# Performance work log

Hardware: AMD Instinct MI355X
Metric: run time of the kernel (lower is better)

The kernel has to match this reference:

```python
import jax, jax.numpy as jnp
import numpy as np
from jax import lax

BETA = 0.1
N_CLUSTERS = 64


def setup_inputs() -> dict:
    key = jax.random.key(0)
    ks = jax.random.split(key, 10)
    L, B, Hin, H = 200, 2048, 64, 256
    s = lambda k, shape, scale=0.05: jax.random.normal(k, shape, dtype=jnp.float32) * scale
    return {
        "X": jax.random.normal(ks[0], (L, B, Hin), dtype=jnp.float32),
        "W_ih0": s(ks[1], (4 * H, Hin)),
        "W_hh0": s(ks[2], (4 * H, H)),
        "b_ih0": s(ks[3], (4 * H,)),
        "b_hh0": s(ks[4], (4 * H,)),
        "W_ih1": s(ks[5], (4 * H, H)),
        "W_hh1": s(ks[6], (4 * H, H)),
        "b_ih1": s(ks[7], (4 * H,)),
        "b_hh1": s(ks[8], (4 * H,)),
        "clusters": jax.random.normal(ks[9], (N_CLUSTERS, H), dtype=jnp.float32),
    }


def _lstm_layer(x, W_ih, W_hh, b_ih, b_hh):
    # x: (L, B, I) -> outputs (L, B, H); torch gate order i, f, g, o
    H = W_hh.shape[1]
    B = x.shape[1]
    b = b_ih + b_hh

    def step(carry, xt):
        h, c = carry
        gates = xt @ W_ih.T + h @ W_hh.T + b  # (B, 4H)
        i, f, g, o = jnp.split(gates, 4, axis=-1)
        c = jax.nn.sigmoid(f) * c + jax.nn.sigmoid(i) * jnp.tanh(g)
        h = jax.nn.sigmoid(o) * jnp.tanh(c)
        return (h, c), h

    h0 = jnp.zeros((B, H), x.dtype)
    (_, _), ys = lax.scan(step, (h0, h0), x)
    return ys


def _encode(X, W_ih0, W_hh0, b_ih0, b_hh0, W_ih1, W_hh1, b_ih1, b_hh1):
    y0 = _lstm_layer(X, W_ih0, W_hh0, b_ih0, b_hh0)
    y1 = _lstm_layer(y0, W_ih1, W_hh1, b_ih1, b_hh1)
    return y1[-1]  # latent_X: (B, H), last timestep of top layer


def reference(X, W_ih0, W_hh0, b_ih0, b_hh0, W_ih1, W_hh1, b_ih1, b_hh1, clusters):
    latent_X = _encode(X, W_ih0, W_hh0, b_ih0, b_hh0, W_ih1, W_hh1, b_ih1, b_hh1)

    # kmeans assignment on detached latents (l2 distance)
    lat_sg = lax.stop_gradient(latent_X)
    d2 = (jnp.sum(lat_sg * lat_sg, -1, keepdims=True)
          - 2.0 * lat_sg @ clusters.T
          + jnp.sum(clusters * clusters, -1))  # (B, K)
    cluster_id = jnp.argmin(d2, axis=-1)  # (B,)

    # centroid update from assigned (detached) points; keep old centroid if empty
    sums = jax.ops.segment_sum(lat_sg, cluster_id, num_segments=N_CLUSTERS)
    counts = jax.ops.segment_sum(jnp.ones((lat_sg.shape[0],), lat_sg.dtype),
                                 cluster_id, num_segments=N_CLUSTERS)
    upd = jnp.where(counts[:, None] > 0, sums / jnp.maximum(counts, 1.0)[:, None], clusters)

    # vectorized per-sample cluster distance loss: sum_i 0.5*beta*||latent_i - c[id_i]||^2
    diff = latent_X - upd[cluster_id]  # gather (B, H)
    dist_loss = 0.5 * BETA * jnp.sum(diff * diff)
    return latent_X, dist_loss
```

## Files before the change

kernel.cpp:

```cpp
#include <hip/hip_runtime.h>
#include <hip/hip_bf16.h>
#include <math.h>

typedef unsigned short u16;
typedef unsigned int u32;
typedef __attribute__((ext_vector_type(8))) __bf16 bf16x8;
typedef __attribute__((ext_vector_type(4))) float f32x4;

#define LSTM_L 200
#define LSTM_B 2048
#define LSTM_HIN 64
#define LSTM_H 256
#define NCLUST 64
#define HALF_BETA 0.05f
#define LDS_BYTES 65536
#define ASSIGN_LDS 135424
#define ASSIGN_BLOCKS 64

__device__ __forceinline__ void gload_lds16(const void* g, void* l) {
    __builtin_amdgcn_global_load_lds(
        (__attribute__((address_space(1))) const void*)g,
        (__attribute__((address_space(3))) void*)l, 16, 0, 0);
}

__device__ __forceinline__ float fast_sigmoid(float x) {
    return __builtin_amdgcn_rcpf(1.f + __expf(-x));
}
__device__ __forceinline__ float fast_tanh(float x) {
    return 2.f * __builtin_amdgcn_rcpf(1.f + __expf(-2.f * x)) - 1.f;
}
__device__ __forceinline__ void wt_store(u32* p, u32 v) {
    __hip_atomic_store(p, v, __ATOMIC_RELAXED, __HIP_MEMORY_SCOPE_AGENT);
}

template<int KIN>
__global__ __launch_bounds__(256) void pack_frag(
    const float* __restrict__ Wih, const float* __restrict__ Whh,
    u16* __restrict__ Wp)
{
    constexpr int NCH = (KIN + LSTM_H) / 32;
    const int total = 1024 * (KIN + LSTM_H);
    for (int i = blockIdx.x * 256 + threadIdx.x; i < total; i += gridDim.x * 256) {
        const int e = i & 7;
        int t = i >> 3;
        const int lane = t & 63; t >>= 6;
        const int nf = t & 1;    t >>= 1;
        const int ch = t % NCH;  t /= NCH;
        const int wn = t & 3;
        const int nb = t >> 2;
        const int l15 = lane & 15;
        const int j = (2 * nf + (l15 & 1)) * 256 + nb * 32 + wn * 8 + (l15 >> 1);
        const int k = ch * 32 + ((lane >> 4) << 3) + e;
        const float v = (k < KIN) ? Wih[(size_t)j * KIN + k]
                                  : Whh[(size_t)j * LSTM_H + (k - KIN)];
        Wp[i] = __builtin_bit_cast(u16, (__bf16)v);
    }
}

template<int KIN>
__device__ __forceinline__ void run_layer64(
    const float* __restrict__ xf32,
    const u16* __restrict__ hbelow,
    const u16* __restrict__ hself,
    const u16* __restrict__ Wp,
    const float* __restrict__ bih, const float* __restrict__ bhh,
    u16* __restrict__ hout, float* __restrict__ latout,
    float* __restrict__ cst,
    int blk, char* smem, int tid)
{
    constexpr int NCH = (KIN + LSTM_H) / 32;
    constexpr bool IS_L0 = (KIN == 64);
    const int lane = tid & 63;
    const int wn = tid >> 6;
    const int l15 = lane & 15;
    const int q = lane >> 4;
    const int mb = blk >> 3;
    const int nb = blk & 7;
    const int b0 = mb * 64;

    bf16x8 Breg[NCH][2];
    {
        const u16* wp = Wp + (size_t)((nb * 4 + wn) * NCH) * 1024 + lane * 8;
#pragma unroll
        for (int ch = 0; ch < NCH; ++ch)
#pragma unroll
            for (int nf = 0; nf < 2; ++nf)
                Breg[ch][nf] = *(const bf16x8*)(wp + (ch * 2 + nf) * 512);
    }

    const int hcol = nb * 32 + wn * 8 + (l15 >> 1);
    float cp[4][4];
#pragma unroll
    for (int mf = 0; mf < 4; ++mf)
#pragma unroll
        for (int r = 0; r < 4; ++r)
            cp[mf][r] = cst[(size_t)(b0 + mf * 16 + q * 4 + r) * 256 + hcol];

    const int gpar = l15 & 1;
    const float b0a = bih[gpar * 256 + hcol] + bhh[gpar * 256 + hcol];
    const float b1a = bih[(2 + gpar) * 256 + hcol] + bhh[(2 + gpar) * 256 + hcol];

    if (IS_L0) {
#pragma unroll
        for (int i = 0; i < 8; ++i) {
            const int slot = i * 256 + tid;
            const int row = slot >> 5;
            const int so = (slot & 31) * 16;
            const int koff = so ^ ((row & 7) << 4);
            gload_lds16((const char*)hself + (size_t)(b0 + row) * 512 + koff,
                        smem + slot * 16);
        }
#pragma unroll
        for (int p = 0; p < 2; ++p) {
            const int slot = p * 256 + tid;
            const int row = slot >> 3;
            const int so = (slot & 7) * 16;
            const int koff = so ^ ((row & 7) << 4);
            const float* s = xf32 + (size_t)(b0 + row) * 64 + (koff >> 1);
            const float4 v0 = *(const float4*)s;
            const float4 v1 = *(const float4*)(s + 4);
            bf16x8 pk;
            pk[0] = (__bf16)v0.x; pk[1] = (__bf16)v0.y;
            pk[2] = (__bf16)v0.z; pk[3] = (__bf16)v0.w;
            pk[4] = (__bf16)v1.x; pk[5] = (__bf16)v1.y;
            pk[6] = (__bf16)v1.z; pk[7] = (__bf16)v1.w;
            *(bf16x8*)(smem + 32768 + slot * 16) = pk;
        }
    } else {
#pragma unroll
        for (int i = 0; i < 16; ++i) {
            const int slot = i * 256 + tid;
            const int row = slot >> 6;
            const int so = (slot & 63) * 16;
            const int koff = so ^ ((row & 7) << 4);
            const char* src = (koff < 512)
                ? (const char*)hbelow + (size_t)(b0 + row) * 512 + koff
                : (const char*)hself + (size_t)(b0 + row) * 512 + (koff - 512);
            gload_lds16(src, smem + slot * 16);
        }
    }
    __syncthreads();

    f32x4 acc[4][2];
#pragma unroll
    for (int mf = 0; mf < 4; ++mf)
#pragma unroll
        for (int nf = 0; nf < 2; ++nf) acc[mf][nf] = f32x4{0.f, 0.f, 0.f, 0.f};

    const int qoff = q * 16;
    const int swzl = (l15 & 7) << 4;
#pragma unroll
    for (int ch = 0; ch < NCH; ++ch) {
        bf16x8 af[4];
#pragma unroll
        for (int mf = 0; mf < 4; ++mf) {
            const int row = mf * 16 + l15;
            const char* ap;
            if (IS_L0) {
                if (ch < 2)
                    ap = smem + 32768 + row * 128 + ((ch * 64 + qoff) ^ swzl);
                else
                    ap = smem + row * 512 + (((ch - 2) * 64 + qoff) ^ swzl);
            } else {
                ap = smem + row * 1024 + ((ch * 64 + qoff) ^ swzl);
            }
            af[mf] = *(const bf16x8*)ap;
        }
#pragma unroll
        for (int mf = 0; mf < 4; ++mf)
#pragma unroll
            for (int nf = 0; nf < 2; ++nf)
                acc[mf][nf] = __builtin_amdgcn_mfma_f32_16x16x32_bf16(
                    af[mf], Breg[ch][nf], acc[mf][nf], 0, 0, 0);
    }

#pragma unroll
    for (int mf = 0; mf < 4; ++mf) {
#pragma unroll
        for (int r = 0; r < 4; ++r) {
            const float a0 = acc[mf][0][r] + b0a;
            const float a1 = acc[mf][1][r] + b1a;
            const float p0 = __shfl_xor(a0, 1);
            const float p1 = __shfl_xor(a1, 1);
            const float gi = gpar ? p0 : a0;
            const float gf = gpar ? a0 : p0;
            const float gg = gpar ? p1 : a1;
            const float go = gpar ? a1 : p1;
            const float cn = fast_sigmoid(gf) * cp[mf][r]
                           + fast_sigmoid(gi) * fast_tanh(gg);
            const float hv = fast_sigmoid(go) * fast_tanh(cn);
            const int rowo = b0 + mf * 16 + q * 4 + r;
            const size_t oidx = (size_t)rowo * 256 + hcol;
            const u16 hb = __builtin_bit_cast(u16, (__bf16)hv);
            const int pr = __shfl_xor((int)(u32)hb, 2);
            const u32 pk = ((u32)hb & 0xffffu) | (((u32)pr) << 16);
            if (gpar) {
                wt_store((u32*)&cst[oidx], __builtin_bit_cast(u32, cn));
            } else if (latout) {
                wt_store((u32*)&latout[oidx], __builtin_bit_cast(u32, hv));
            } else if ((l15 & 3) == 0) {
                wt_store((u32*)hout + ((size_t)rowo * 128 + (hcol >> 1)), pk);
            }
        }
    }
}

__global__ __launch_bounds__(256, 2) void lstm_slot(
    const float* __restrict__ xt,
    const u16* __restrict__ h0c, u16* __restrict__ h0n, float* __restrict__ c0,
    const u16* __restrict__ Wp0,
    const float* __restrict__ bih0, const float* __restrict__ bhh0,
    const u16* __restrict__ h1c, u16* __restrict__ h1n, float* __restrict__ c1,
    const u16* __restrict__ Wp1,
    const float* __restrict__ bih1, const float* __restrict__ bhh1,
    float* __restrict__ latout, int do0, int do1)
{
    extern __shared__ char smem[];
    const int tid = threadIdx.x;
    if (blockIdx.x < 256) {
        if (do0)
            run_layer64<LSTM_HIN>(xt, nullptr, h0c, Wp0, bih0, bhh0,
                                  h0n, nullptr, c0, blockIdx.x, smem, tid);
    } else {
        if (do1)
            run_layer64<LSTM_H>(nullptr, h0c, h1c, Wp1, bih1, bhh1,
                                h1n, latout, c1, blockIdx.x - 256, smem, tid);
    }
}

__global__ __launch_bounds__(256, 1) void assign_fused(
    const float* __restrict__ lat, const float* __restrict__ clusters,
    int* __restrict__ ids, float* __restrict__ partial, int* __restrict__ pcount)
{
    extern __shared__ char sm[];
    float* clT    = (float*)sm;
    float* psum   = (float*)(sm + 65536);
    float* rowbuf = (float*)(sm + 131072);
    int*   pcnt   = (int*)(sm + 135168);

    const int tid = threadIdx.x;
    const int k = tid & 63;
    const int w = tid >> 6;

    for (int i = tid; i < 16384; i += 256) {
        const int kk = i >> 8, j = i & 255;
        clT[j * 64 + kk] = clusters[(size_t)kk * 256 + j];
        psum[i] = 0.f;
    }
    if (tid < 64) pcnt[tid] = 0;
    __syncthreads();

    float* rb = rowbuf + w * 256;
    const int rbase = (int)blockIdx.x * 32 + w * 8;
    for (int rr = 0; rr < 8; ++rr) {
        const int row = rbase + rr;
#pragma unroll
        for (int p = 0; p < 4; ++p)
            rb[p * 64 + k] = lat[(size_t)row * 256 + p * 64 + k];
        float d0 = 0.f, d1 = 0.f, d2 = 0.f, d3 = 0.f;
#pragma unroll 4
        for (int j = 0; j < 256; j += 4) {
            const float t0 = rb[j + 0] - clT[(j + 0) * 64 + k];
            const float t1 = rb[j + 1] - clT[(j + 1) * 64 + k];
            const float t2 = rb[j + 2] - clT[(j + 2) * 64 + k];
            const float t3 = rb[j + 3] - clT[(j + 3) * 64 + k];
            d0 += t0 * t0; d1 += t1 * t1; d2 += t2 * t2; d3 += t3 * t3;
        }
        float d = (d0 + d1) + (d2 + d3);
        int idx = k;
        for (int off = 32; off > 0; off >>= 1) {
            const float od = __shfl_down(d, off, 64);
            const int   oi = __shfl_down(idx, off, 64);
            if (od < d || (od == d && oi < idx)) { d = od; idx = oi; }
        }
        const int best = __shfl(idx, 0, 64);
        if (k == 0) { ids[row] = best; atomicAdd(&pcnt[best], 1); }
#pragma unroll
        for (int p = 0; p < 4; ++p)
            atomicAdd(&psum[best * 256 + p * 64 + k], rb[p * 64 + k]);
    }
    __syncthreads();
    for (int i = tid; i < 16384; i += 256)
        partial[(size_t)blockIdx.x * 16384 + i] = psum[i];
    if (tid < 64) pcount[(size_t)blockIdx.x * 64 + tid] = pcnt[tid];
}

__global__ __launch_bounds__(256) void centroid_final2(
    const float* __restrict__ partial, const int* __restrict__ pcount,
    const float* __restrict__ clusters, float* __restrict__ upd)
{
    const int k = blockIdx.x;
    const int h = threadIdx.x;
    float s = 0.f;
    int c = 0;
    for (int b = 0; b < ASSIGN_BLOCKS; ++b) {
        s += partial[(size_t)b * 16384 + k * 256 + h];
        c += pcount[(size_t)b * 64 + k];
    }
    upd[(size_t)k * LSTM_H + h] = (c > 0)
        ? s / (float)c
        : clusters[(size_t)k * LSTM_H + h];
}

__global__ __launch_bounds__(256) void loss_kernel(
    const float* __restrict__ lat, const int* __restrict__ ids,
    const float* __restrict__ upd, float* __restrict__ out_loss)
{
    float p = 0.f;
    const int total = LSTM_B * LSTM_H;
    for (int idx = blockIdx.x * blockDim.x + threadIdx.x; idx < total;
         idx += gridDim.x * blockDim.x) {
        const int b = idx >> 8;
        const float d = lat[idx] - upd[(size_t)ids[b] * LSTM_H + (idx & 255)];
        p += d * d;
    }
    for (int off = 32; off > 0; off >>= 1) p += __shfl_down(p, off, 64);
    __shared__ float wsum[4];
    const int lane = threadIdx.x & 63, wid = threadIdx.x >> 6;
    if (lane == 0) wsum[wid] = p;
    __syncthreads();
    if (threadIdx.x == 0)
        atomicAdd(out_loss, HALF_BETA * (wsum[0] + wsum[1] + wsum[2] + wsum[3]));
}

extern "C" void kernel_launch(void* const* d_in, const int* in_sizes, int n_in,
                              void* d_out, int out_size, void* d_ws, size_t ws_size,
                              hipStream_t stream)
{
    const float* X     = (const float*)d_in[0];
    const float* Wih0  = (const float*)d_in[1];
    const float* Whh0  = (const float*)d_in[2];
    const float* bih0  = (const float*)d_in[3];
    const float* bhh0  = (const float*)d_in[4];
    const float* Wih1  = (const float*)d_in[5];
    const float* Whh1  = (const float*)d_in[6];
    const float* bih1  = (const float*)d_in[7];
    const float* bhh1  = (const float*)d_in[8];
    const float* clust = (const float*)d_in[9];

    float* out = (float*)d_out;
    char* base = (char*)d_ws;
    const size_t MB = 1u << 20;
    const size_t KB = 1024;

    u16* Wp0      = (u16*)(base + 0 * MB);
    u16* Wp1      = (u16*)(base + 1 * MB);
    u16* h0a      = (u16*)(base + 2 * MB);
    u16* h0b      = (u16*)(base + 3 * MB);
    u16* h1a      = (u16*)(base + 4 * MB);
    u16* h1b      = (u16*)(base + 5 * MB);
    float* c0     = (float*)(base + 6 * MB);
    float* c1     = (float*)(base + 8 * MB);
    float* partial= (float*)(base + 6 * MB);
    float* upd    = (float*)(base + 10 * MB);
    int* pcount   = (int*)(base + 10 * MB + 64 * KB);
    int* ids      = (int*)(base + 10 * MB + 80 * KB);

    const size_t BH = (size_t)LSTM_B * LSTM_H;

    hipMemsetAsync(h0a, 0, MB, stream);
    hipMemsetAsync(h1a, 0, MB, stream);
    hipMemsetAsync(c0, 0, 4 * MB, stream);
    hipMemsetAsync(out + BH, 0, sizeof(float), stream);

    pack_frag<LSTM_HIN><<<320, 256, 0, stream>>>(Wih0, Whh0, Wp0);
    pack_frag<LSTM_H>  <<<512, 256, 0, stream>>>(Wih1, Whh1, Wp1);

    hipFuncSetAttribute((const void*)lstm_slot,
                        hipFuncAttributeMaxDynamicSharedMemorySize, LDS_BYTES);
    hipFuncSetAttribute((const void*)assign_fused,
                        hipFuncAttributeMaxDynamicSharedMemorySize, ASSIGN_LDS);

    u16* h0c = h0a; u16* h0n = h0b;
    u16* h1c = h1a; u16* h1n = h1b;
    for (int s = 0; s <= LSTM_L; ++s) {
        const int do0 = (s < LSTM_L) ? 1 : 0;
        const int do1 = (s > 0) ? 1 : 0;
        const float* xt = do0 ? X + (size_t)s * LSTM_B * LSTM_HIN : nullptr;
        float* lat = (s == LSTM_L) ? out : nullptr;
        lstm_slot<<<512, 256, LDS_BYTES, stream>>>(
            xt, h0c, h0n, c0, Wp0, bih0, bhh0,
            h1c, h1n, c1, Wp1, bih1, bhh1, lat, do0, do1);
        if (do0) { u16* t = h0c; h0c = h0n; h0n = t; }
        if (do1) { u16* t = h1c; h1c = h1n; h1n = t; }
    }

    assign_fused<<<ASSIGN_BLOCKS, 256, ASSIGN_LDS, stream>>>(
        out, clust, ids, partial, pcount);
    centroid_final2<<<NCLUST, 256, 0, stream>>>(partial, pcount, clust, upd);
    loss_kernel<<<256, 256, 0, stream>>>(out, ids, upd, out + BH);
}
```

Before: 2.456 ms.

## Compute k-means loss algebraically and replace memsets with one zero-init kernel

The distance loss is rewritten as sum||x||^2 minus sum over clusters of ||S_k||^2/n_k. The row norms are accumulated inside the assignment kernel and the correction is applied in a small finalize kernel, so the ids buffer, the upd buffer and the gather-based loss kernel are no longer needed. The four memsets become a single zero-init kernel, and the cell-state memset is replaced by a 'first step' flag that starts the carry at zero instead of reading it. The algebraic form trades the direct difference for a subtraction of two large sums, which can lose floating-point precision.

```diff
diff --git a/kernel.cpp b/kernel.cpp
--- a/kernel.cpp
+++ b/kernel.cpp
@@ -31,6 +31,14 @@
 }
 __device__ __forceinline__ void wt_store(u32* p, u32 v) {
     __hip_atomic_store(p, v, __ATOMIC_RELAXED, __HIP_MEMORY_SCOPE_AGENT);
+}
+
+__global__ __launch_bounds__(256) void zero_init(
+    u32* __restrict__ h0a, u32* __restrict__ h1a, float* __restrict__ loss)
+{
+    const int t = blockIdx.x * 256 + threadIdx.x;
+    for (int i = t; i < 262144; i += 65536) { h0a[i] = 0u; h1a[i] = 0u; }
+    if (t == 0) *loss = 0.f;
 }
 
 template<int KIN>
@@ -65,7 +73,7 @@
     const u16* __restrict__ Wp,
     const float* __restrict__ bih, const float* __restrict__ bhh,
     u16* __restrict__ hout, float* __restrict__ latout,
-    float* __restrict__ cst,
+    float* __restrict__ cst, int first,
     int blk, char* smem, int tid)
 {
     constexpr int NCH = (KIN + LSTM_H) / 32;
@@ -90,11 +98,18 @@
 
     const int hcol = nb * 32 + wn * 8 + (l15 >> 1);
     float cp[4][4];
-#pragma unroll
-    for (int mf = 0; mf < 4; ++mf)
-#pragma unroll
-        for (int r = 0; r < 4; ++r)
-            cp[mf][r] = cst[(size_t)(b0 + mf * 16 + q * 4 + r) * 256 + hcol];
+    if (first) {
+#pragma unroll
+        for (int mf = 0; mf < 4; ++mf)
+#pragma unroll
+            for (int r = 0; r < 4; ++r) cp[mf][r] = 0.f;
+    } else {
+#pragma unroll
+        for (int mf = 0; mf < 4; ++mf)
+#pragma unroll
+            for (int r = 0; r < 4; ++r)
+                cp[mf][r] = cst[(size_t)(b0 + mf * 16 + q * 4 + r) * 256 + hcol];
+    }
 
     const int gpar = l15 & 1;
     const float b0a = bih[gpar * 256 + hcol] + bhh[gpar * 256 + hcol];
@@ -213,30 +228,32 @@
     const u16* __restrict__ h1c, u16* __restrict__ h1n, float* __restrict__ c1,
     const u16* __restrict__ Wp1,
     const float* __restrict__ bih1, const float* __restrict__ bhh1,
-    float* __restrict__ latout, int do0, int do1)
+    float* __restrict__ latout, int do0, int do1, int first0, int first1)
 {
     extern __shared__ char smem[];
     const int tid = threadIdx.x;
     if (blockIdx.x < 256) {
         if (do0)
             run_layer64<LSTM_HIN>(xt, nullptr, h0c, Wp0, bih0, bhh0,
-                                  h0n, nullptr, c0, blockIdx.x, smem, tid);
+                                  h0n, nullptr, c0, first0, blockIdx.x, smem, tid);
     } else {
         if (do1)
             run_layer64<LSTM_H>(nullptr, h0c, h1c, Wp1, bih1, bhh1,
-                                h1n, latout, c1, blockIdx.x - 256, smem, tid);
+                                h1n, latout, c1, first1, blockIdx.x - 256, smem, tid);
     }
 }
 
 __global__ __launch_bounds__(256, 1) void assign_fused(
     const float* __restrict__ lat, const float* __restrict__ clusters,
-    int* __restrict__ ids, float* __restrict__ partial, int* __restrict__ pcount)
+    float* __restrict__ partial, int* __restrict__ pcount,
+    float* __restrict__ out_loss)
 {
     extern __shared__ char sm[];
     float* clT    = (float*)sm;
     float* psum   = (float*)(sm + 65536);
     float* rowbuf = (float*)(sm + 131072);
     int*   pcnt   = (int*)(sm + 135168);
+    __shared__ float xw[4];
 
     const int tid = threadIdx.x;
     const int k = tid & 63;
@@ -252,11 +269,15 @@
 
     float* rb = rowbuf + w * 256;
     const int rbase = (int)blockIdx.x * 32 + w * 8;
+    float xs = 0.f;
     for (int rr = 0; rr < 8; ++rr) {
         const int row = rbase + rr;
 #pragma unroll
-        for (int p = 0; p < 4; ++p)
-            rb[p * 64 + k] = lat[(size_t)row * 256 + p * 64 + k];
+        for (int p = 0; p < 4; ++p) {
+            const float v = lat[(size_t)row * 256 + p * 64 + k];
+            rb[p * 64 + k] = v;
+            xs += v * v;
+        }
         float d0 = 0.f, d1 = 0.f, d2 = 0.f, d3 = 0.f;
 #pragma unroll 4
         for (int j = 0; j < 256; j += 4) {
@@ -274,53 +295,43 @@
             if (od < d || (od == d && oi < idx)) { d = od; idx = oi; }
         }
         const int best = __shfl(idx, 0, 64);
-        if (k == 0) { ids[row] = best; atomicAdd(&pcnt[best], 1); }
+        if (k == 0) atomicAdd(&pcnt[best], 1);
 #pragma unroll
         for (int p = 0; p < 4; ++p)
             atomicAdd(&psum[best * 256 + p * 64 + k], rb[p * 64 + k]);
     }
+    for (int off = 32; off > 0; off >>= 1) xs += __shfl_down(xs, off, 64);
+    if (k == 0) xw[w] = xs;
     __syncthreads();
+    if (tid == 0)
+        atomicAdd(out_loss, HALF_BETA * (xw[0] + xw[1] + xw[2] + xw[3]));
     for (int i = tid; i < 16384; i += 256)
         partial[(size_t)blockIdx.x * 16384 + i] = psum[i];
     if (tid < 64) pcount[(size_t)blockIdx.x * 64 + tid] = pcnt[tid];
 }
 
-__global__ __launch_bounds__(256) void centroid_final2(
+__global__ __launch_bounds__(256) void finalize_loss(
     const float* __restrict__ partial, const int* __restrict__ pcount,
-    const float* __restrict__ clusters, float* __restrict__ upd)
+    float* __restrict__ out_loss)
 {
     const int k = blockIdx.x;
     const int h = threadIdx.x;
     float s = 0.f;
+    for (int b = 0; b < ASSIGN_BLOCKS; ++b)
+        s += partial[(size_t)b * 16384 + k * 256 + h];
     int c = 0;
-    for (int b = 0; b < ASSIGN_BLOCKS; ++b) {
-        s += partial[(size_t)b * 16384 + k * 256 + h];
+    for (int b = 0; b < ASSIGN_BLOCKS; ++b)
         c += pcount[(size_t)b * 64 + k];
-    }
-    upd[(size_t)k * LSTM_H + h] = (c > 0)
-        ? s / (float)c
-        : clusters[(size_t)k * LSTM_H + h];
-}
-
-__global__ __launch_bounds__(256) void loss_kernel(
-    const float* __restrict__ lat, const int* __restrict__ ids,
-    const float* __restrict__ upd, float* __restrict__ out_loss)
-{
-    float p = 0.f;
-    const int total = LSTM_B * LSTM_H;
-    for (int idx = blockIdx.x * blockDim.x + threadIdx.x; idx < total;
-         idx += gridDim.x * blockDim.x) {
-        const int b = idx >> 8;
-        const float d = lat[idx] - upd[(size_t)ids[b] * LSTM_H + (idx & 255)];
-        p += d * d;
-    }
-    for (int off = 32; off > 0; off >>= 1) p += __shfl_down(p, off, 64);
+    float ss = s * s;
+    for (int off = 32; off > 0; off >>= 1) ss += __shfl_down(ss, off, 64);
     __shared__ float wsum[4];
-    const int lane = threadIdx.x & 63, wid = threadIdx.x >> 6;
-    if (lane == 0) wsum[wid] = p;
+    const int lane = h & 63, wid = h >> 6;
+    if (lane == 0) wsum[wid] = ss;
     __syncthreads();
-    if (threadIdx.x == 0)
-        atomicAdd(out_loss, HALF_BETA * (wsum[0] + wsum[1] + wsum[2] + wsum[3]));
+    if (h == 0 && c > 0) {
+        const float tot = wsum[0] + wsum[1] + wsum[2] + wsum[3];
+        atomicAdd(out_loss, -HALF_BETA * tot / (float)c);
+    }
 }
 
 extern "C" void kernel_launch(void* const* d_in, const int* in_sizes, int n_in,
@@ -352,17 +363,11 @@
     float* c0     = (float*)(base + 6 * MB);
     float* c1     = (float*)(base + 8 * MB);
     float* partial= (float*)(base + 6 * MB);
-    float* upd    = (float*)(base + 10 * MB);
-    int* pcount   = (int*)(base + 10 * MB + 64 * KB);
-    int* ids      = (int*)(base + 10 * MB + 80 * KB);
+    int* pcount   = (int*)(base + 10 * MB);
 
     const size_t BH = (size_t)LSTM_B * LSTM_H;
 
-    hipMemsetAsync(h0a, 0, MB, stream);
-    hipMemsetAsync(h1a, 0, MB, stream);
-    hipMemsetAsync(c0, 0, 4 * MB, stream);
-    hipMemsetAsync(out + BH, 0, sizeof(float), stream);
-
+    zero_init<<<256, 256, 0, stream>>>((u32*)h0a, (u32*)h1a, out + BH);
     pack_frag<LSTM_HIN><<<320, 256, 0, stream>>>(Wih0, Whh0, Wp0);
     pack_frag<LSTM_H>  <<<512, 256, 0, stream>>>(Wih1, Whh1, Wp1);
 
@@ -376,17 +381,18 @@
     for (int s = 0; s <= LSTM_L; ++s) {
         const int do0 = (s < LSTM_L) ? 1 : 0;
         const int do1 = (s > 0) ? 1 : 0;
+        const int first0 = (s == 0) ? 1 : 0;
+        const int first1 = (s == 1) ? 1 : 0;
         const float* xt = do0 ? X + (size_t)s * LSTM_B * LSTM_HIN : nullptr;
         float* lat = (s == LSTM_L) ? out : nullptr;
         lstm_slot<<<512, 256, LDS_BYTES, stream>>>(
             xt, h0c, h0n, c0, Wp0, bih0, bhh0,
-            h1c, h1n, c1, Wp1, bih1, bhh1, lat, do0, do1);
+            h1c, h1n, c1, Wp1, bih1, bhh1, lat, do0, do1, first0, first1);
         if (do0) { u16* t = h0c; h0c = h0n; h0n = t; }
         if (do1) { u16* t = h1c; h1c = h1n; h1n = t; }
     }
 
     assign_fused<<<ASSIGN_BLOCKS, 256, ASSIGN_LDS, stream>>>(
-        out, clust, ids, partial, pcount);
-    centroid_final2<<<NCLUST, 256, 0, stream>>>(partial, pcount, clust, upd);
-    loss_kernel<<<256, 256, 0, stream>>>(out, ids, upd, out + BH);
-}
+        out, clust, partial, pcount, out + BH);
+    finalize_loss<<<NCLUST, 256, 0, stream>>>(partial, pcount, out + BH);
+}
```

After: 2.515 ms. 1.02x slower.
